# Kernel optimization log

Measured on AMD Instinct MI355X. Metric: run time of the kernel, lower is better.

Reference implementation:

```python
import jax, jax.numpy as jnp
import numpy as np

D_IN = 768      # residual-stream width
D_SAE = 16384   # dictionary size
T = 4           # positions per window
K = 64          # TopK sparsity
PREFIX = (8192, 16384)  # prefix_sum for n_scales=2 even split
B = 1024


def setup_inputs() -> dict:
    key = jax.random.key(0)
    ks = jax.random.split(key, 6)
    x = jax.random.normal(ks[0], (B, T, D_IN), jnp.float32)
    # encoder weight ~ kaiming-uniform scale
    W_enc = jax.random.normal(ks[1], (T, D_IN, D_SAE), jnp.float32) * (1.0 / np.sqrt(D_IN))
    b_enc = jnp.zeros((D_SAE,), jnp.float32)
    # per-scale decoders, row-normalized over (T, d_in) as in _normalize_decoder
    def make_dec(k, prefix):
        W = jax.random.normal(k, (prefix, T, D_IN), jnp.float32)
        norms = jnp.linalg.norm(W.reshape(prefix, -1), axis=1).clip(1e-8)
        return W / norms[:, None, None]
    W_dec0 = make_dec(ks[2], PREFIX[0])
    W_dec1 = make_dec(ks[3], PREFIX[1])
    b_dec0 = jnp.zeros((T, D_IN), jnp.float32)
    b_dec1 = jnp.zeros((T, D_IN), jnp.float32)
    # non-identity per-position prefix permutation (T, d_sae)
    perm_keys = jax.random.split(ks[4], T)
    pos_prefix_perm = jax.vmap(lambda k: jax.random.permutation(k, D_SAE))(perm_keys).astype(jnp.int32)
    return {
        'x': x, 'W_enc': W_enc, 'b_enc': b_enc,
        'W_dec0': W_dec0, 'b_dec0': b_dec0,
        'W_dec1': W_dec1, 'b_dec1': b_dec1,
        'pos_prefix_perm': pos_prefix_perm,
    }


def reference(x, W_enc, b_enc, W_dec0, b_dec0, W_dec1, b_dec1, pos_prefix_perm):
    # ---- encode: pre-activation + per-row TopK + ReLU scatter into sparse code z
    pre = jnp.einsum('btd,tds->bs', x, W_enc) + b_enc            # (B, d_sae)
    vals, idx = jax.lax.top_k(pre, K)                            # (B, K)
    b = pre.shape[0]
    z = jnp.zeros_like(pre).at[jnp.arange(b)[:, None], idx].set(jax.nn.relu(vals))
    # ---- matryoshka per-(position, scale) reconstruction loss
    total = jnp.asarray(0.0, pre.dtype)
    x_hat_full = None
    for W, bd in ((W_dec0, b_dec0), (W_dec1, b_dec1)):
        prefix = W.shape[0]
        # position-dependent permutation gather: z_g[b,t,p] = z[b, perm[t,p]]
        z_g = z[:, pos_prefix_perm[:, :prefix]]                  # (B, T, prefix)
        x_hat = jnp.einsum('btp,ptd->btd', z_g, W) + bd          # (B, T, d_in)
        # sum over t of mean_b sum_d err^2  (== loop over t in the original)
        total = total + jnp.sum(jnp.mean(jnp.sum((x_hat - x) ** 2, axis=-1), axis=0))
        x_hat_full = x_hat
    total = total / (T * 2)  # divide by T * n_scales
    # aux-k loss: freshly initialized module has no dead latents
    # (num_tokens_since_fired starts at 0 << dead_threshold_tokens), so l_auxk == 0.
    return total, x_hat_full, z
```

## Files before the change

### kernel.cpp

```cpp
#include <hip/hip_runtime.h>
#include <hip/hip_bf16.h>
#include <stdint.h>

#define NB    1024
#define NT    4
#define NDIN  768
#define NSAE  16384
#define NK    64
#define KDIM  3072
#define PFX0  8192
#define KT96  96
#define VKD   6144

typedef _Float16 f16x8 __attribute__((ext_vector_type(8)));
typedef _Float16 f16x4 __attribute__((ext_vector_type(4)));
typedef float    f32x4 __attribute__((ext_vector_type(4)));

__device__ __forceinline__ unsigned f2key(float f) {
    union { float f; unsigned u; } cv; cv.f = f;
    unsigned u = cv.u;
    return u ^ ((unsigned)((int)u >> 31) | 0x80000000u);
}

__device__ __forceinline__ void ld16(const _Float16* g, _Float16* l) {
    __builtin_amdgcn_global_load_lds(
        (const __attribute__((address_space(1))) void*)g,
        (__attribute__((address_space(3))) void*)l, 16, 0, 0);
}

__global__ __launch_bounds__(256) void conv_a_kernel(
    const float* __restrict__ A, _Float16* __restrict__ A2)
{
    const int gid = blockIdx.x * 256 + threadIdx.x;
    const int m = gid / (KDIM / 4);
    const int k = (gid % (KDIM / 4)) * 4;
    const float4 v = *(const float4*)(A + (size_t)m * KDIM + k);
    const float vv[4] = { v.x, v.y, v.z, v.w };
    f16x4 h, l;
#pragma unroll
    for (int j = 0; j < 4; ++j) {
        const float sv = vv[j] * 64.f;
        const _Float16 hh = (_Float16)sv;
        h[j] = hh;
        l[j] = (_Float16)(sv - (float)hh);
    }
    const size_t ob = (size_t)m * VKD + (k >> 5) * 64 + (k & 31);
    *(f16x4*)(A2 + ob)      = h;
    *(f16x4*)(A2 + ob + 32) = l;
}

__global__ __launch_bounds__(256) void conv_bt_kernel(
    const float* __restrict__ B, _Float16* __restrict__ B2)
{
    __shared__ float ts[64][65];
    const int n0 = blockIdx.x * 64;
    const int k0 = blockIdx.y * 64;
    const int tid = threadIdx.x;
#pragma unroll
    for (int i = 0; i < 4; ++i) {
        const int r = (tid >> 4) + i * 16;
        const int c = (tid & 15) * 4;
        const float4 v = *(const float4*)(B + (size_t)(k0 + r) * NSAE + n0 + c);
        ts[r][c] = v.x; ts[r][c + 1] = v.y; ts[r][c + 2] = v.z; ts[r][c + 3] = v.w;
    }
    __syncthreads();
    const int part = tid & 15;
    const int vk = part * 8;
    const int chunk = vk >> 6;
    const int off = vk & 63;
    const bool lo = off >= 32;
    const int kb = chunk * 32 + (off & 31);
#pragma unroll
    for (int g = 0; g < 4; ++g) {
        const int nl = (tid >> 4) + g * 16;
        f16x8 o;
#pragma unroll
        for (int j = 0; j < 8; ++j) {
            const float sv = ts[kb + j][nl] * 64.f;
            const _Float16 hh = (_Float16)sv;
            o[j] = lo ? (_Float16)(sv - (float)hh) : hh;
        }
        const size_t ob = (size_t)(n0 + nl) * VKD + (size_t)(k0 >> 5) * 64 + vk;
        *(f16x8*)(B2 + ob) = o;
    }
}

__global__ __launch_bounds__(512, 2) void gemm_f16split_kernel(
    const _Float16* __restrict__ A2, const _Float16* __restrict__ B2,
    const float* __restrict__ bias, float* __restrict__ pre)
{
    __shared__ _Float16 sA[2 * 256 * 64];
    __shared__ _Float16 sB[2 * 256 * 64];
    const int tid = threadIdx.x;
    const int lane = tid & 63;
    const int wid = tid >> 6;
    const int wm = wid >> 2;
    const int wn = wid & 3;

    const int bid = blockIdx.x;
    const int swz = (bid & 7) * 32 + (bid >> 3);
    const int m0 = (swz & 3) * 256;
    const int n0 = (swz >> 2) * 256;

    const _Float16* pa[4]; const _Float16* pb[4];
    _Float16* da[4]; _Float16* db[4];
#pragma unroll
    for (int r = 0; r < 4; ++r) {
        const int d = tid + r * 512;
        const int row = d >> 3;
        const int ls = (d & 7) ^ (row & 7);
        pa[r] = A2 + (size_t)(m0 + row) * VKD + ls * 8;
        pb[r] = B2 + (size_t)(n0 + row) * VKD + ls * 8;
        da[r] = sA + d * 8;
        db[r] = sB + d * 8;
    }

    const int rl = lane & 15;
    const int qw = lane >> 4;
    const int aoff0 = ((0 + qw) ^ (rl & 7)) * 8 + rl * 64;
    const int aoff1 = ((4 + qw) ^ (rl & 7)) * 8 + rl * 64;

    f32x4 acc[8][4];
#pragma unroll
    for (int mi = 0; mi < 8; ++mi)
#pragma unroll
        for (int ni = 0; ni < 4; ++ni)
            acc[mi][ni] = (f32x4){0.f, 0.f, 0.f, 0.f};

#pragma unroll
    for (int r = 0; r < 4; ++r) { ld16(pa[r], da[r]); ld16(pb[r], db[r]); }

    for (int kt = 0; kt < KT96; ++kt) {
        const int cb = (kt & 1) ? 16384 : 0;
        const int nb = cb ^ 16384;
        if (kt + 1 < KT96) {
            const int ko = (kt + 1) * 64;
#pragma unroll
            for (int r = 0; r < 4; ++r) {
                ld16(pa[r] + ko, da[r] + nb);
                ld16(pb[r] + ko, db[r] + nb);
            }
            asm volatile("s_waitcnt vmcnt(8)" ::: "memory");
        } else {
            asm volatile("s_waitcnt vmcnt(0)" ::: "memory");
        }
        __builtin_amdgcn_sched_barrier(0);
        __builtin_amdgcn_s_barrier();
        __builtin_amdgcn_sched_barrier(0);

        __builtin_amdgcn_s_setprio(1);
        f16x8 bf[4][2];
#pragma unroll
        for (int ni = 0; ni < 4; ++ni) {
            const int rb = cb + (wn * 64 + ni * 16) * 64;
            bf[ni][0] = *(const f16x8*)(sB + rb + aoff0);
            bf[ni][1] = *(const f16x8*)(sB + rb + aoff1);
        }
#pragma unroll
        for (int h = 0; h < 2; ++h) {
            f16x8 af[4][2];
#pragma unroll
            for (int i = 0; i < 4; ++i) {
                const int ra = cb + (wm * 128 + (h * 4 + i) * 16) * 64;
                af[i][0] = *(const f16x8*)(sA + ra + aoff0);
                af[i][1] = *(const f16x8*)(sA + ra + aoff1);
            }
#pragma unroll
            for (int i = 0; i < 4; ++i)
#pragma unroll
                for (int ni = 0; ni < 4; ++ni) {
                    acc[h * 4 + i][ni] = __builtin_amdgcn_mfma_f32_16x16x32_f16(af[i][0], bf[ni][0], acc[h * 4 + i][ni], 0, 0, 0);
                    acc[h * 4 + i][ni] = __builtin_amdgcn_mfma_f32_16x16x32_f16(af[i][0], bf[ni][1], acc[h * 4 + i][ni], 0, 0, 0);
                    acc[h * 4 + i][ni] = __builtin_amdgcn_mfma_f32_16x16x32_f16(af[i][1], bf[ni][0], acc[h * 4 + i][ni], 0, 0, 0);
                }
        }
        __builtin_amdgcn_s_setprio(0);
        __builtin_amdgcn_sched_barrier(0);
        __builtin_amdgcn_s_barrier();
    }

    const float c12 = 1.0f / 4096.0f;
    float bv[4];
#pragma unroll
    for (int ni = 0; ni < 4; ++ni) bv[ni] = bias[n0 + wn * 64 + ni * 16 + rl];
#pragma unroll
    for (int mi = 0; mi < 8; ++mi)
#pragma unroll
        for (int ni = 0; ni < 4; ++ni)
#pragma unroll
            for (int r = 0; r < 4; ++r) {
                const int row = m0 + wm * 128 + mi * 16 + qw * 4 + r;
                const int col = n0 + wn * 64 + ni * 16 + rl;
                pre[(size_t)row * NSAE + col] = acc[mi][ni][r] * c12 + bv[ni];
            }
}

__global__ __launch_bounds__(256) void gemm_pre_kernel(
    const float* __restrict__ A, const float* __restrict__ Bm,
    const float* __restrict__ bias, float* __restrict__ pre)
{
    __shared__ float As[16][128];
    __shared__ float Bs[16][128];
    const int bn = blockIdx.x * 128;
    const int bm = blockIdx.y * 128;
    const int tid = threadIdx.x;
    const int tx = tid & 15;
    const int ty = tid >> 4;

    float acc[8][8];
#pragma unroll
    for (int i = 0; i < 8; ++i)
#pragma unroll
        for (int j = 0; j < 8; ++j) acc[i][j] = 0.f;

    for (int k0 = 0; k0 < KDIM; k0 += 16) {
#pragma unroll
        for (int i = 0; i < 2; ++i) {
            const int idx = i * 256 + tid;
            const int r = idx >> 2;
            const int c = (idx & 3) << 2;
            const float4 v = *(const float4*)(A + (size_t)(bm + r) * KDIM + (k0 + c));
            As[c + 0][r] = v.x; As[c + 1][r] = v.y;
            As[c + 2][r] = v.z; As[c + 3][r] = v.w;
        }
#pragma unroll
        for (int i = 0; i < 2; ++i) {
            const int idx = i * 256 + tid;
            const int r = idx >> 5;
            const int c = (idx & 31) << 2;
            *(float4*)(&Bs[r][c]) = *(const float4*)(Bm + (size_t)(k0 + r) * NSAE + (bn + c));
        }
        __syncthreads();
#pragma unroll
        for (int kk = 0; kk < 16; ++kk) {
            const float4 a0 = *(const float4*)(&As[kk][ty * 8]);
            const float4 a1 = *(const float4*)(&As[kk][ty * 8 + 4]);
            const float4 b0 = *(const float4*)(&Bs[kk][tx * 8]);
            const float4 b1 = *(const float4*)(&Bs[kk][tx * 8 + 4]);
            const float av[8] = { a0.x, a0.y, a0.z, a0.w, a1.x, a1.y, a1.z, a1.w };
            const float bv[8] = { b0.x, b0.y, b0.z, b0.w, b1.x, b1.y, b1.z, b1.w };
#pragma unroll
            for (int i = 0; i < 8; ++i)
#pragma unroll
                for (int j = 0; j < 8; ++j)
                    acc[i][j] = fmaf(av[i], bv[j], acc[i][j]);
        }
        __syncthreads();
    }

    float bv8[8];
#pragma unroll
    for (int j = 0; j < 8; ++j) bv8[j] = bias[bn + tx * 8 + j];
#pragma unroll
    for (int i = 0; i < 8; ++i) {
        float4 o0, o1;
        o0.x = acc[i][0] + bv8[0]; o0.y = acc[i][1] + bv8[1];
        o0.z = acc[i][2] + bv8[2]; o0.w = acc[i][3] + bv8[3];
        o1.x = acc[i][4] + bv8[4]; o1.y = acc[i][5] + bv8[5];
        o1.z = acc[i][6] + bv8[6]; o1.w = acc[i][7] + bv8[7];
        const size_t off = (size_t)(bm + ty * 8 + i) * NSAE + bn + tx * 8;
        *(float4*)(pre + off) = o0;
        *(float4*)(pre + off + 4) = o1;
    }
}

__global__ __launch_bounds__(256) void topk_kernel(
    const float* __restrict__ pre,
    int* __restrict__ tk_idx, float* __restrict__ tk_val,
    float* __restrict__ z)
{
    __shared__ unsigned hist[4][256];
    __shared__ int sel[NK];
    __shared__ float sval[NK];
    __shared__ int ties[256];
    __shared__ float tval[256];
    __shared__ unsigned sh_prefix, sh_want, sh_cnt, sh_tiecnt;

    const int b = blockIdx.x;
    const int tid = threadIdx.x;
    const int w = tid >> 6;
    const float* row = pre + (size_t)b * NSAE;
    float* zrow = z + (size_t)b * NSAE;

    if (tid == 0) { sh_prefix = 0u; sh_want = NK; sh_cnt = 0u; sh_tiecnt = 0u; }
    hist[0][tid] = 0u; hist[1][tid] = 0u; hist[2][tid] = 0u; hist[3][tid] = 0u;
    __syncthreads();

    float4 rv[16];
#pragma unroll
    for (int j = 0; j < 16; ++j) {
        const int i = tid * 4 + j * 1024;
        rv[j] = *(const float4*)(row + i);
        *(float4*)(zrow + i) = make_float4(0.f, 0.f, 0.f, 0.f);
        atomicAdd(&hist[w][f2key(rv[j].x) >> 24], 1u);
        atomicAdd(&hist[w][f2key(rv[j].y) >> 24], 1u);
        atomicAdd(&hist[w][f2key(rv[j].z) >> 24], 1u);
        atomicAdd(&hist[w][f2key(rv[j].w) >> 24], 1u);
    }
    __syncthreads();
    hist[0][tid] += hist[1][tid] + hist[2][tid] + hist[3][tid];
    __syncthreads();
    if (tid == 0) {
        unsigned cum = 0u; int bsel = 0;
        for (int bin = 255; bin >= 0; --bin) {
            const unsigned c = hist[0][bin];
            if (cum + c >= NK) { bsel = bin; break; }
            cum += c;
        }
        sh_prefix = ((unsigned)bsel << 24);
        sh_want = NK - cum;
    }
    __syncthreads();

    for (int pass = 1; pass < 4; ++pass) {
        hist[0][tid] = 0u; hist[1][tid] = 0u; hist[2][tid] = 0u; hist[3][tid] = 0u;
        __syncthreads();
        const int shift = 24 - pass * 8;
        const unsigned mask = 0xFFFFFFFFu << (shift + 8);
        const unsigned pfx = sh_prefix;
#pragma unroll
        for (int j = 0; j < 16; ++j) {
            const float fv[4] = { rv[j].x, rv[j].y, rv[j].z, rv[j].w };
#pragma unroll
            for (int q = 0; q < 4; ++q) {
                const unsigned k = f2key(fv[q]);
                if ((k & mask) == pfx) atomicAdd(&hist[w][(k >> shift) & 0xFFu], 1u);
            }
        }
        __syncthreads();
        hist[0][tid] += hist[1][tid] + hist[2][tid] + hist[3][tid];
        __syncthreads();
        if (tid == 0) {
            const unsigned want = sh_want;
            unsigned cum = 0u; int bsel = 0;
            for (int bin = 255; bin >= 0; --bin) {
                const unsigned c = hist[0][bin];
                if (cum + c >= want) { bsel = bin; break; }
                cum += c;
            }
            sh_prefix |= ((unsigned)bsel << shift);
            sh_want = want - cum;
        }
        __syncthreads();
    }

    const unsigned T = sh_prefix;
#pragma unroll
    for (int j = 0; j < 16; ++j) {
        const float fv[4] = { rv[j].x, rv[j].y, rv[j].z, rv[j].w };
#pragma unroll
        for (int q = 0; q < 4; ++q) {
            const unsigned k = f2key(fv[q]);
            if (k > T) {
                const unsigned s = atomicAdd(&sh_cnt, 1u);
                sel[s] = tid * 4 + j * 1024 + q;
                sval[s] = fv[q];
            } else if (k == T) {
                const unsigned s = atomicAdd(&sh_tiecnt, 1u);
                if (s < 256u) { ties[s] = tid * 4 + j * 1024 + q; tval[s] = fv[q]; }
            }
        }
    }
    __syncthreads();
    if (tid == 0) {
        const unsigned tc = sh_tiecnt;
        const int n = (int)(tc < 256u ? tc : 256u);
        for (int a = 1; a < n; ++a) {
            const int v = ties[a]; const float fv = tval[a]; int c = a;
            while (c > 0 && ties[c - 1] > v) {
                ties[c] = ties[c - 1]; tval[c] = tval[c - 1]; --c;
            }
            ties[c] = v; tval[c] = fv;
        }
        const int base = (int)sh_cnt;
        const int want = (int)sh_want;
        for (int j = 0; j < want && j < n; ++j) {
            sel[base + j] = ties[j]; sval[base + j] = tval[j];
        }
    }
    __syncthreads();
    if (tid < NK) {
        const int myi = sel[tid];
        int rank = 0;
#pragma unroll 1
        for (int j = 0; j < NK; ++j) rank += (sel[j] < myi) ? 1 : 0;
        const float v = fmaxf(sval[tid], 0.f);
        tk_idx[b * NK + rank] = myi;
        tk_val[b * NK + rank] = v;
        zrow[myi] = v;
    }
}

__global__ __launch_bounds__(256) void invperm_kernel(
    const int* __restrict__ perm, int* __restrict__ ipos)
{
    const int i = blockIdx.x * 256 + threadIdx.x;
    if (i < NT * NSAE) {
        const int t = i >> 14;
        ipos[t * NSAE + perm[i]] = i & (NSAE - 1);
    }
}

__global__ __launch_bounds__(256) void decode_kernel(
    const float* __restrict__ x,
    const int* __restrict__ tk_idx, const float* __restrict__ tk_val,
    const int* __restrict__ ipos,
    const float* __restrict__ Wd0, const float* __restrict__ bd0,
    const float* __restrict__ Wd1, const float* __restrict__ bd1,
    float* __restrict__ xhat, float* __restrict__ part0, float* __restrict__ part1)
{
    const int gbid = blockIdx.x;
    const int t = gbid >> 10;
    const int b = gbid & (NB - 1);
    const int bt = b * NT + t;
    const int tid = threadIdx.x;

    __shared__ int s_p[NK];
    __shared__ float s_v[NK];
    if (tid < NK) {
        const int s = tk_idx[b * NK + tid];
        s_v[tid] = tk_val[b * NK + tid];
        s_p[tid] = ipos[t * NSAE + s];
    }
    __syncthreads();

    float acc0[3], acc1[3];
#pragma unroll
    for (int r = 0; r < 3; ++r) {
        const int d = tid + 256 * r;
        acc0[r] = bd0[t * NDIN + d];
        acc1[r] = bd1[t * NDIN + d];
    }
    for (int j = 0; j < NK; ++j) {
        const int p = s_p[j];
        const float v = s_v[j];
        const float* w1 = Wd1 + ((size_t)p * NT + t) * NDIN;
#pragma unroll
        for (int r = 0; r < 3; ++r) acc1[r] = fmaf(v, w1[tid + 256 * r], acc1[r]);
        if (p < PFX0) {
            const float* w0 = Wd0 + ((size_t)p * NT + t) * NDIN;
#pragma unroll
            for (int r = 0; r < 3; ++r) acc0[r] = fmaf(v, w0[tid + 256 * r], acc0[r]);
        }
    }

    float e0 = 0.f, e1 = 0.f;
#pragma unroll
    for (int r = 0; r < 3; ++r) {
        const int d = tid + 256 * r;
        const float xv = x[(size_t)bt * NDIN + d];
        const float d0 = acc0[r] - xv;
        const float d1 = acc1[r] - xv;
        e0 = fmaf(d0, d0, e0);
        e1 = fmaf(d1, d1, e1);
        xhat[(size_t)bt * NDIN + d] = acc1[r];
    }

    __shared__ float r0[256];
    __shared__ float r1[256];
    r0[tid] = e0; r1[tid] = e1;
    __syncthreads();
    for (int w = 128; w > 0; w >>= 1) {
        if (tid < w) { r0[tid] += r0[tid + w]; r1[tid] += r1[tid + w]; }
        __syncthreads();
    }
    if (tid == 0) { part0[bt] = r0[0]; part1[bt] = r1[0]; }
}

__global__ __launch_bounds__(256) void reduce_kernel(
    const float* __restrict__ part0, const float* __restrict__ part1,
    float* __restrict__ out_total)
{
    __shared__ double red[256];
    const int tid = threadIdx.x;
    double s = 0.0;
    for (int i = tid; i < NB * NT; i += 256)
        s += (double)part0[i] + (double)part1[i];
    red[tid] = s;
    __syncthreads();
    for (int w = 128; w > 0; w >>= 1) {
        if (tid < w) red[tid] += red[tid + w];
        __syncthreads();
    }
    if (tid == 0) out_total[0] = (float)(red[0] / ((double)NB * (double)(NT * 2)));
}

extern "C" void kernel_launch(void* const* d_in, const int* in_sizes, int n_in,
                              void* d_out, int out_size, void* d_ws, size_t ws_size,
                              hipStream_t stream)
{
    const float* x     = (const float*)d_in[0];
    const float* W_enc = (const float*)d_in[1];
    const float* b_enc = (const float*)d_in[2];
    const float* Wd0   = (const float*)d_in[3];
    const float* bd0   = (const float*)d_in[4];
    const float* Wd1   = (const float*)d_in[5];
    const float* bd1   = (const float*)d_in[6];
    const int*   perm  = (const int*)d_in[7];

    float* out       = (float*)d_out;
    float* out_total = out;
    float* out_xhat  = out + 1;
    float* out_z     = out + 1 + (size_t)NB * NT * NDIN;

    char* ws = (char*)d_ws;
    size_t off = 0;
    float* pre = (float*)(ws + off); off += (size_t)NB * NSAE * sizeof(float);

    const size_t szA2 = (size_t)NB * VKD * sizeof(_Float16);
    const size_t szB2 = (size_t)NSAE * VKD * sizeof(_Float16);
    _Float16* A2 = (_Float16*)(ws + off);
    _Float16* B2 = (_Float16*)(ws + off + szA2);
    const size_t off_splits_end = off + szA2 + szB2;

    const bool fast = (ws_size >= off_splits_end +
        ((size_t)NB * NK * 8 + (size_t)NT * NSAE * 4 + (size_t)NB * NT * 8));
    size_t tail = fast ? off_splits_end : off;
    int*   tk_idx = (int*)(ws + tail);   tail += (size_t)NB * NK * sizeof(int);
    float* tk_val = (float*)(ws + tail); tail += (size_t)NB * NK * sizeof(float);
    int*   ipos   = (int*)(ws + tail);   tail += (size_t)NT * NSAE * sizeof(int);
    float* part0  = (float*)(ws + tail); tail += (size_t)NB * NT * sizeof(float);
    float* part1  = (float*)(ws + tail);

    if (fast) {
        conv_a_kernel<<<(NB * KDIM) / (256 * 4), 256, 0, stream>>>(x, A2);
        conv_bt_kernel<<<dim3(NSAE / 64, KDIM / 64), 256, 0, stream>>>(W_enc, B2);
        gemm_f16split_kernel<<<256, 512, 0, stream>>>(A2, B2, b_enc, pre);
    } else {
        gemm_pre_kernel<<<dim3(NSAE / 128, NB / 128), 256, 0, stream>>>(x, W_enc, b_enc, pre);
    }
    invperm_kernel<<<(NT * NSAE) / 256, 256, 0, stream>>>(perm, ipos);
    topk_kernel<<<NB, 256, 0, stream>>>(pre, tk_idx, tk_val, out_z);
    decode_kernel<<<NB * NT, 256, 0, stream>>>(x, tk_idx, tk_val, ipos,
                                               Wd0, bd0, Wd1, bd1,
                                               out_xhat, part0, part1);
    reduce_kernel<<<1, 256, 0, stream>>>(part0, part1, out_total);
}
```

Baseline: 613.1 us.

## Split GEMM k-step into four phases interleaving LDS reads, prefetch and MFMA

Restructures the main loop of the encoder GEMM into four phases. Each phase reads a slice of A fragments from LDS, issues part of the next tile's global-to-LDS prefetch (A in phase 0, B in phase 1), then runs the MFMAs for two M-subtiles. The aim is to spread memory traffic across the MFMA work instead of bunching it at the start of each k-step. In exchange it adds block barriers per phase and waits for vmcnt(0) at the end of each iteration, which may expose global load latency that the previous vmcnt(8) scheme hid.

After: 617.6 us. About the same (+0.7%).

```diff
diff --git a/kernel.cpp b/kernel.cpp
--- a/kernel.cpp
+++ b/kernel.cpp
@@ -85,6 +85,35 @@
     }
 }
 
+#define READ_A(af, mibase)                                                   \
+    _Pragma("unroll")                                                        \
+    for (int i = 0; i < 2; ++i) {                                            \
+        const int ra = cb + (wm * 128 + ((mibase) + i) * 16) * 64;           \
+        af[i][0] = *(const f16x8*)(sA + ra + aoff0);                         \
+        af[i][1] = *(const f16x8*)(sA + ra + aoff1);                         \
+    }
+
+#define PHASE_MFMA(p, af)                                                    \
+    _Pragma("unroll")                                                        \
+    for (int i = 0; i < 2; ++i)                                              \
+        _Pragma("unroll")                                                    \
+        for (int ni = 0; ni < 4; ++ni) {                                     \
+            acc[(p) * 2 + i][ni] = __builtin_amdgcn_mfma_f32_16x16x32_f16(af[i][0], bf[ni][0], acc[(p) * 2 + i][ni], 0, 0, 0); \
+            acc[(p) * 2 + i][ni] = __builtin_amdgcn_mfma_f32_16x16x32_f16(af[i][0], bf[ni][1], acc[(p) * 2 + i][ni], 0, 0, 0); \
+            acc[(p) * 2 + i][ni] = __builtin_amdgcn_mfma_f32_16x16x32_f16(af[i][1], bf[ni][0], acc[(p) * 2 + i][ni], 0, 0, 0); \
+        }
+
+#define PHASE_TAIL()                                                         \
+    __builtin_amdgcn_s_barrier();                                            \
+    asm volatile("s_waitcnt lgkmcnt(0)" ::: "memory");                       \
+    __builtin_amdgcn_sched_barrier(0);                                       \
+    __builtin_amdgcn_s_setprio(1);
+
+#define PHASE_END()                                                          \
+    __builtin_amdgcn_s_setprio(0);                                           \
+    __builtin_amdgcn_sched_barrier(0);                                       \
+    __builtin_amdgcn_s_barrier();
+
 __global__ __launch_bounds__(512, 2) void gemm_f16split_kernel(
     const _Float16* __restrict__ A2, const _Float16* __restrict__ B2,
     const float* __restrict__ bias, float* __restrict__ pre)
@@ -129,26 +158,16 @@
 
 #pragma unroll
     for (int r = 0; r < 4; ++r) { ld16(pa[r], da[r]); ld16(pb[r], db[r]); }
+    asm volatile("s_waitcnt vmcnt(0)" ::: "memory");
+    __builtin_amdgcn_sched_barrier(0);
+    __builtin_amdgcn_s_barrier();
 
     for (int kt = 0; kt < KT96; ++kt) {
         const int cb = (kt & 1) ? 16384 : 0;
         const int nb = cb ^ 16384;
-        if (kt + 1 < KT96) {
-            const int ko = (kt + 1) * 64;
-#pragma unroll
-            for (int r = 0; r < 4; ++r) {
-                ld16(pa[r] + ko, da[r] + nb);
-                ld16(pb[r] + ko, db[r] + nb);
-            }
-            asm volatile("s_waitcnt vmcnt(8)" ::: "memory");
-        } else {
-            asm volatile("s_waitcnt vmcnt(0)" ::: "memory");
-        }
-        __builtin_amdgcn_sched_barrier(0);
-        __builtin_amdgcn_s_barrier();
-        __builtin_amdgcn_sched_barrier(0);
-
-        __builtin_amdgcn_s_setprio(1);
+        const bool pf = (kt + 1 < KT96);
+        const int ko = (kt + 1) * 64;
+
         f16x8 bf[4][2];
 #pragma unroll
         for (int ni = 0; ni < 4; ++ni) {
@@ -156,25 +175,38 @@
             bf[ni][0] = *(const f16x8*)(sB + rb + aoff0);
             bf[ni][1] = *(const f16x8*)(sB + rb + aoff1);
         }
-#pragma unroll
-        for (int h = 0; h < 2; ++h) {
-            f16x8 af[4][2];
-#pragma unroll
-            for (int i = 0; i < 4; ++i) {
-                const int ra = cb + (wm * 128 + (h * 4 + i) * 16) * 64;
-                af[i][0] = *(const f16x8*)(sA + ra + aoff0);
-                af[i][1] = *(const f16x8*)(sA + ra + aoff1);
-            }
-#pragma unroll
-            for (int i = 0; i < 4; ++i)
-#pragma unroll
-                for (int ni = 0; ni < 4; ++ni) {
-                    acc[h * 4 + i][ni] = __builtin_amdgcn_mfma_f32_16x16x32_f16(af[i][0], bf[ni][0], acc[h * 4 + i][ni], 0, 0, 0);
-                    acc[h * 4 + i][ni] = __builtin_amdgcn_mfma_f32_16x16x32_f16(af[i][0], bf[ni][1], acc[h * 4 + i][ni], 0, 0, 0);
-                    acc[h * 4 + i][ni] = __builtin_amdgcn_mfma_f32_16x16x32_f16(af[i][1], bf[ni][0], acc[h * 4 + i][ni], 0, 0, 0);
-                }
-        }
+        f16x8 af0[2][2];
+        READ_A(af0, 0)
+        if (pf) {
+            ld16(pa[0] + ko, da[0] + nb); ld16(pa[1] + ko, da[1] + nb);
+            ld16(pa[2] + ko, da[2] + nb); ld16(pa[3] + ko, da[3] + nb);
+        }
+        PHASE_TAIL()
+        PHASE_MFMA(0, af0)
+        PHASE_END()
+
+        f16x8 af1[2][2];
+        READ_A(af1, 2)
+        if (pf) {
+            ld16(pb[0] + ko, db[0] + nb); ld16(pb[1] + ko, db[1] + nb);
+            ld16(pb[2] + ko, db[2] + nb); ld16(pb[3] + ko, db[3] + nb);
+        }
+        PHASE_TAIL()
+        PHASE_MFMA(1, af1)
+        PHASE_END()
+
+        f16x8 af2[2][2];
+        READ_A(af2, 4)
+        PHASE_TAIL()
+        PHASE_MFMA(2, af2)
+        PHASE_END()
+
+        f16x8 af3[2][2];
+        READ_A(af3, 6)
+        PHASE_TAIL()
+        PHASE_MFMA(3, af3)
         __builtin_amdgcn_s_setprio(0);
+        asm volatile("s_waitcnt vmcnt(0)" ::: "memory");
         __builtin_amdgcn_sched_barrier(0);
         __builtin_amdgcn_s_barrier();
     }
```

## Split decode top-k loop across wavefronts with float4 loads and LDS reduction

Applied to the files above, without the earlier changes.

The decode kernel now gives each of the four wavefronts 16 of the 64 selected latents instead of having every thread walk all 64. Each lane loads decoder rows as float4, and the four partial sums are combined through shared memory before the bias, error and output step. The goal is more memory-level parallelism and wider loads in the gather-heavy decode. In exchange it adds 24 KB of LDS, which may reduce occupancy, plus an extra barrier and reduction pass.

Result: no change. 624.4 us (+1.8%).

```diff
diff --git a/kernel.cpp b/kernel.cpp
--- a/kernel.cpp
+++ b/kernel.cpp
@@ -414,9 +414,13 @@
     const int b = gbid & (NB - 1);
     const int bt = b * NT + t;
     const int tid = threadIdx.x;
+    const int w = tid >> 6;
+    const int lane = tid & 63;
 
     __shared__ int s_p[NK];
     __shared__ float s_v[NK];
+    __shared__ float red0[4][NDIN];
+    __shared__ float red1[4][NDIN];
     if (tid < NK) {
         const int s = tk_idx[b * NK + tid];
         s_v[tid] = tk_val[b * NK + tid];
@@ -424,47 +428,69 @@
     }
     __syncthreads();
 
-    float acc0[3], acc1[3];
+    f32x4 a0[3], a1[3];
+#pragma unroll
+    for (int r = 0; r < 3; ++r) {
+        a0[r] = (f32x4){0.f, 0.f, 0.f, 0.f};
+        a1[r] = (f32x4){0.f, 0.f, 0.f, 0.f};
+    }
+    const int j0 = w * 16;
+    for (int j = j0; j < j0 + 16; ++j) {
+        const int p = s_p[j];
+        const float v = s_v[j];
+        const float4* w1 = (const float4*)(Wd1 + ((size_t)p * NT + t) * NDIN);
+#pragma unroll
+        for (int r = 0; r < 3; ++r) {
+            const float4 f = w1[lane + 64 * r];
+            a1[r][0] = fmaf(v, f.x, a1[r][0]);
+            a1[r][1] = fmaf(v, f.y, a1[r][1]);
+            a1[r][2] = fmaf(v, f.z, a1[r][2]);
+            a1[r][3] = fmaf(v, f.w, a1[r][3]);
+        }
+        if (p < PFX0) {
+            const float4* w0 = (const float4*)(Wd0 + ((size_t)p * NT + t) * NDIN);
+#pragma unroll
+            for (int r = 0; r < 3; ++r) {
+                const float4 f = w0[lane + 64 * r];
+                a0[r][0] = fmaf(v, f.x, a0[r][0]);
+                a0[r][1] = fmaf(v, f.y, a0[r][1]);
+                a0[r][2] = fmaf(v, f.z, a0[r][2]);
+                a0[r][3] = fmaf(v, f.w, a0[r][3]);
+            }
+        }
+    }
+#pragma unroll
+    for (int r = 0; r < 3; ++r) {
+        *(f32x4*)(&red0[w][4 * (lane + 64 * r)]) = a0[r];
+        *(f32x4*)(&red1[w][4 * (lane + 64 * r)]) = a1[r];
+    }
+    __syncthreads();
+
+    float e0 = 0.f, e1 = 0.f;
 #pragma unroll
     for (int r = 0; r < 3; ++r) {
         const int d = tid + 256 * r;
-        acc0[r] = bd0[t * NDIN + d];
-        acc1[r] = bd1[t * NDIN + d];
-    }
-    for (int j = 0; j < NK; ++j) {
-        const int p = s_p[j];
-        const float v = s_v[j];
-        const float* w1 = Wd1 + ((size_t)p * NT + t) * NDIN;
-#pragma unroll
-        for (int r = 0; r < 3; ++r) acc1[r] = fmaf(v, w1[tid + 256 * r], acc1[r]);
-        if (p < PFX0) {
-            const float* w0 = Wd0 + ((size_t)p * NT + t) * NDIN;
-#pragma unroll
-            for (int r = 0; r < 3; ++r) acc0[r] = fmaf(v, w0[tid + 256 * r], acc0[r]);
-        }
-    }
-
-    float e0 = 0.f, e1 = 0.f;
-#pragma unroll
-    for (int r = 0; r < 3; ++r) {
-        const int d = tid + 256 * r;
+        const float v0 = bd0[t * NDIN + d] +
+            ((red0[0][d] + red0[1][d]) + (red0[2][d] + red0[3][d]));
+        const float v1 = bd1[t * NDIN + d] +
+            ((red1[0][d] + red1[1][d]) + (red1[2][d] + red1[3][d]));
         const float xv = x[(size_t)bt * NDIN + d];
-        const float d0 = acc0[r] - xv;
-        const float d1 = acc1[r] - xv;
+        const float d0 = v0 - xv;
+        const float d1 = v1 - xv;
         e0 = fmaf(d0, d0, e0);
         e1 = fmaf(d1, d1, e1);
-        xhat[(size_t)bt * NDIN + d] = acc1[r];
-    }
-
-    __shared__ float r0[256];
-    __shared__ float r1[256];
-    r0[tid] = e0; r1[tid] = e1;
-    __syncthreads();
-    for (int w = 128; w > 0; w >>= 1) {
-        if (tid < w) { r0[tid] += r0[tid + w]; r1[tid] += r1[tid + w]; }
-        __syncthreads();
-    }
-    if (tid == 0) { part0[bt] = r0[0]; part1[bt] = r1[0]; }
+        xhat[(size_t)bt * NDIN + d] = v1;
+    }
+
+    __shared__ float r0s[256];
+    __shared__ float r1s[256];
+    r0s[tid] = e0; r1s[tid] = e1;
+    __syncthreads();
+    for (int s = 128; s > 0; s >>= 1) {
+        if (tid < s) { r0s[tid] += r0s[tid + s]; r1s[tid] += r1s[tid + s]; }
+        __syncthreads();
+    }
+    if (tid == 0) { part0[bt] = r0s[0]; part1[bt] = r1s[0]; }
 }
 
 __global__ __launch_bounds__(256) void reduce_kernel(
```

## Fuse W_enc fp16 split conversion into GEMM B-tile loading

Applied to the files above, without the earlier changes.

Removes the separate conv_bt pre-pass that transposed W_enc and split it into hi/lo fp16 halves in a workspace buffer. The GEMM now streams fp32 W_enc tiles straight into LDS with an XOR swizzle and does the split per fragment in registers. This drops a full write and reread of the converted weight buffer and one kernel launch. The cost is extra conversion ALU work and scalar strided LDS reads inside the GEMM main loop.

After: 593.0 us. 3.3% less time.

```diff
diff --git a/kernel.cpp b/kernel.cpp
--- a/kernel.cpp
+++ b/kernel.cpp
@@ -22,7 +22,7 @@
     return u ^ ((unsigned)((int)u >> 31) | 0x80000000u);
 }
 
-__device__ __forceinline__ void ld16(const _Float16* g, _Float16* l) {
+__device__ __forceinline__ void ld16(const void* g, void* l) {
     __builtin_amdgcn_global_load_lds(
         (const __attribute__((address_space(1))) void*)g,
         (__attribute__((address_space(3))) void*)l, 16, 0, 0);
@@ -49,48 +49,12 @@
     *(f16x4*)(A2 + ob + 32) = l;
 }
 
-__global__ __launch_bounds__(256) void conv_bt_kernel(
-    const float* __restrict__ B, _Float16* __restrict__ B2)
-{
-    __shared__ float ts[64][65];
-    const int n0 = blockIdx.x * 64;
-    const int k0 = blockIdx.y * 64;
-    const int tid = threadIdx.x;
-#pragma unroll
-    for (int i = 0; i < 4; ++i) {
-        const int r = (tid >> 4) + i * 16;
-        const int c = (tid & 15) * 4;
-        const float4 v = *(const float4*)(B + (size_t)(k0 + r) * NSAE + n0 + c);
-        ts[r][c] = v.x; ts[r][c + 1] = v.y; ts[r][c + 2] = v.z; ts[r][c + 3] = v.w;
-    }
-    __syncthreads();
-    const int part = tid & 15;
-    const int vk = part * 8;
-    const int chunk = vk >> 6;
-    const int off = vk & 63;
-    const bool lo = off >= 32;
-    const int kb = chunk * 32 + (off & 31);
-#pragma unroll
-    for (int g = 0; g < 4; ++g) {
-        const int nl = (tid >> 4) + g * 16;
-        f16x8 o;
-#pragma unroll
-        for (int j = 0; j < 8; ++j) {
-            const float sv = ts[kb + j][nl] * 64.f;
-            const _Float16 hh = (_Float16)sv;
-            o[j] = lo ? (_Float16)(sv - (float)hh) : hh;
-        }
-        const size_t ob = (size_t)(n0 + nl) * VKD + (size_t)(k0 >> 5) * 64 + vk;
-        *(f16x8*)(B2 + ob) = o;
-    }
-}
-
 __global__ __launch_bounds__(512, 2) void gemm_f16split_kernel(
-    const _Float16* __restrict__ A2, const _Float16* __restrict__ B2,
+    const _Float16* __restrict__ A2, const float* __restrict__ Bsrc,
     const float* __restrict__ bias, float* __restrict__ pre)
 {
     __shared__ _Float16 sA[2 * 256 * 64];
-    __shared__ _Float16 sB[2 * 256 * 64];
+    __shared__ float    sB32[2 * 32 * 256];
     const int tid = threadIdx.x;
     const int lane = tid & 63;
     const int wid = tid >> 6;
@@ -102,17 +66,20 @@
     const int m0 = (swz & 3) * 256;
     const int n0 = (swz >> 2) * 256;
 
-    const _Float16* pa[4]; const _Float16* pb[4];
-    _Float16* da[4]; _Float16* db[4];
+    const _Float16* pa[4]; const float* pb[4];
+    _Float16* da[4]; float* db[4];
 #pragma unroll
     for (int r = 0; r < 4; ++r) {
         const int d = tid + r * 512;
-        const int row = d >> 3;
-        const int ls = (d & 7) ^ (row & 7);
-        pa[r] = A2 + (size_t)(m0 + row) * VKD + ls * 8;
-        pb[r] = B2 + (size_t)(n0 + row) * VKD + ls * 8;
+        const int rowA = d >> 3;
+        const int lsA = (d & 7) ^ (rowA & 7);
+        pa[r] = A2 + (size_t)(m0 + rowA) * VKD + lsA * 8;
         da[r] = sA + d * 8;
-        db[r] = sB + d * 8;
+        const int kB = d >> 6;
+        const int slotB = d & 63;
+        const int gk = (kB & 7) ^ (((kB >> 3) & 3) << 2);
+        pb[r] = Bsrc + (size_t)kB * NSAE + n0 + ((slotB ^ gk) << 2);
+        db[r] = sB32 + d * 4;
     }
 
     const int rl = lane & 15;
@@ -130,15 +97,20 @@
 #pragma unroll
     for (int r = 0; r < 4; ++r) { ld16(pa[r], da[r]); ld16(pb[r], db[r]); }
 
+    const size_t KSTRB = (size_t)32 * NSAE;
+
     for (int kt = 0; kt < KT96; ++kt) {
-        const int cb = (kt & 1) ? 16384 : 0;
-        const int nb = cb ^ 16384;
+        const int cbA = (kt & 1) ? 16384 : 0;
+        const int nbA = cbA ^ 16384;
+        const int cbB = (kt & 1) ? 8192 : 0;
+        const int nbB = cbB ^ 8192;
         if (kt + 1 < KT96) {
-            const int ko = (kt + 1) * 64;
+            const int koA = (kt + 1) * 64;
+            const size_t koB = (size_t)(kt + 1) * KSTRB;
 #pragma unroll
             for (int r = 0; r < 4; ++r) {
-                ld16(pa[r] + ko, da[r] + nb);
-                ld16(pb[r] + ko, db[r] + nb);
+                ld16(pa[r] + koA, da[r] + nbA);
+                ld16(pb[r] + koB, db[r] + nbB);
             }
             asm volatile("s_waitcnt vmcnt(8)" ::: "memory");
         } else {
@@ -152,16 +124,30 @@
         f16x8 bf[4][2];
 #pragma unroll
         for (int ni = 0; ni < 4; ++ni) {
-            const int rb = cb + (wn * 64 + ni * 16) * 64;
-            bf[ni][0] = *(const f16x8*)(sB + rb + aoff0);
-            bf[ni][1] = *(const f16x8*)(sB + rb + aoff1);
+            const int nslot = wn * 16 + ni * 4 + (rl >> 2);
+            const int s0 = nslot ^ (qw << 2);
+            const int base = cbB + (qw * 8) * 256 + (rl & 3);
+            float fv[8];
+#pragma unroll
+            for (int j = 0; j < 8; ++j)
+                fv[j] = sB32[base + j * 256 + ((s0 ^ j) << 2)];
+            f16x8 h, l;
+#pragma unroll
+            for (int j = 0; j < 8; ++j) {
+                const float sv = fv[j] * 64.f;
+                const _Float16 hh = (_Float16)sv;
+                h[j] = hh;
+                l[j] = (_Float16)(sv - (float)hh);
+            }
+            bf[ni][0] = h;
+            bf[ni][1] = l;
         }
 #pragma unroll
         for (int h = 0; h < 2; ++h) {
             f16x8 af[4][2];
 #pragma unroll
             for (int i = 0; i < 4; ++i) {
-                const int ra = cb + (wm * 128 + (h * 4 + i) * 16) * 64;
+                const int ra = cbA + (wm * 128 + (h * 4 + i) * 16) * 64;
                 af[i][0] = *(const f16x8*)(sA + ra + aoff0);
                 af[i][1] = *(const f16x8*)(sA + ra + aoff1);
             }
@@ -508,10 +494,8 @@
     float* pre = (float*)(ws + off); off += (size_t)NB * NSAE * sizeof(float);
 
     const size_t szA2 = (size_t)NB * VKD * sizeof(_Float16);
-    const size_t szB2 = (size_t)NSAE * VKD * sizeof(_Float16);
     _Float16* A2 = (_Float16*)(ws + off);
-    _Float16* B2 = (_Float16*)(ws + off + szA2);
-    const size_t off_splits_end = off + szA2 + szB2;
+    const size_t off_splits_end = off + szA2;
 
     const bool fast = (ws_size >= off_splits_end +
         ((size_t)NB * NK * 8 + (size_t)NT * NSAE * 4 + (size_t)NB * NT * 8));
@@ -524,8 +508,7 @@
 
     if (fast) {
         conv_a_kernel<<<(NB * KDIM) / (256 * 4), 256, 0, stream>>>(x, A2);
-        conv_bt_kernel<<<dim3(NSAE / 64, KDIM / 64), 256, 0, stream>>>(W_enc, B2);
-        gemm_f16split_kernel<<<256, 512, 0, stream>>>(A2, B2, b_enc, pre);
+        gemm_f16split_kernel<<<256, 512, 0, stream>>>(A2, W_enc, b_enc, pre);
     } else {
         gemm_pre_kernel<<<dim3(NSAE / 128, NB / 128), 256, 0, stream>>>(x, W_enc, b_enc, pre);
     }
```
